# Optimization experiments

Measured on AMD Instinct MI355X. Metric: run time of the kernel, lower is better.

The kernel has to match this reference:

```python
import jax, jax.numpy as jnp
import numpy as np

N = 100000
E = 1600000
D_IN = 128
D_OUT = 128
EPS = 1e-5


def setup_inputs() -> dict:
    key = jax.random.key(0)
    ks = jax.random.split(key, 8)
    x = jax.random.normal(ks[0], (N, D_IN), dtype=jnp.float32)
    edge_index = jax.random.randint(ks[1], (2, E), 0, N, dtype=jnp.int64)
    s1 = 1.0 / np.sqrt(D_IN)
    s2 = 1.0 / np.sqrt(D_OUT)
    W1 = jax.random.uniform(ks[2], (D_IN, D_OUT), jnp.float32, -s1, s1)
    b1 = jax.random.uniform(ks[3], (D_OUT,), jnp.float32, -s1, s1)
    W2 = jax.random.uniform(ks[4], (D_OUT, D_OUT), jnp.float32, -s2, s2)
    b2 = jax.random.uniform(ks[5], (D_OUT,), jnp.float32, -s2, s2)
    gamma = jnp.ones((D_OUT,), jnp.float32)
    beta = jnp.zeros((D_OUT,), jnp.float32)
    return {"x": x, "edge_index": edge_index, "W1": W1, "b1": b1,
            "W2": W2, "b2": b2, "gamma": gamma, "beta": beta}


def reference(x, edge_index, W1, b1, W2, b2, gamma, beta):
    row, col = edge_index[0], edge_index[1]
    # scatter-add neighbor aggregation: agg[row] += x[col]
    agg = jax.ops.segment_sum(x[col], row, num_segments=N)
    h = x + agg  # residual (self) + aggregated neighbors
    # MLP: Linear -> ReLU -> Linear -> BatchNorm1d (training-mode batch stats)
    h = jax.nn.relu(h @ W1 + b1)
    h = h @ W2 + b2
    mean = jnp.mean(h, axis=0)
    var = jnp.mean(jnp.square(h - mean), axis=0)  # biased var, as torch BN uses
    out = gamma * (h - mean) * jax.lax.rsqrt(var + EPS) + beta
    return out
```

## Files before the change

### kernel.cpp

```cpp
#include <hip/hip_runtime.h>

#define N_NODES 100000
#define N_EDGES 1600000
#define DIM     128
#define EPS_BN  1e-5f
#define NB      512
#define NPB     196
#define EPB     3125
#define CAP     4096
#define M_TILE  64
#define M_PAD   100032
#define GBLK    1563
#define LPITCH  136

typedef __attribute__((ext_vector_type(8))) short short8;
typedef __attribute__((ext_vector_type(4))) float floatx4;

__device__ __forceinline__ unsigned short f2bf(float f) {
    unsigned u = __float_as_uint(f);
    return (unsigned short)((u + 0x7FFF + ((u >> 16) & 1)) >> 16);
}
__device__ __forceinline__ float bf2f(unsigned short b) {
    return __uint_as_float((unsigned)b << 16);
}

__device__ __forceinline__ int detect64(const void* eidx) {
    int v = ((const int*)eidx)[2 * (threadIdx.x & 63) + 1];
    unsigned long long b = __ballot(v != 0);
    return (b == 0ULL) ? 1 : 0;
}

__device__ __forceinline__ int load_row(const void* eidx, int is64, int e) {
    if (is64) return (int)((const long long*)eidx)[e];
    return ((const int*)eidx)[e];
}
__device__ __forceinline__ int load_col(const void* eidx, int is64, int e) {
    if (is64) return (int)((const long long*)eidx)[N_EDGES + e];
    return ((const int*)eidx)[N_EDGES + e];
}

__global__ __launch_bounds__(256) void bin_scatter(const void* eidx, int* bcur,
                                                   uint2* slots) {
    __shared__ int lh[NB];
    __shared__ int lbase[NB];
    for (int i = threadIdx.x; i < NB; i += 256) lh[i] = 0;
    int is64 = detect64(eidx);
    __syncthreads();
    int base = blockIdx.x * EPB;
    for (int i = threadIdx.x; i < EPB; i += 256) {
        int r = load_row(eidx, is64, base + i);
        atomicAdd(&lh[r / NPB], 1);
    }
    __syncthreads();
    for (int i = threadIdx.x; i < NB; i += 256) {
        int c = lh[i];
        lbase[i] = c ? atomicAdd(&bcur[i], c) : 0;
        lh[i] = 0;
    }
    __syncthreads();
    for (int i = threadIdx.x; i < EPB; i += 256) {
        int r = load_row(eidx, is64, base + i);
        int c = load_col(eidx, is64, base + i);
        int b = r / NPB;
        int pos = lbase[b] + atomicAdd(&lh[b], 1);
        slots[b * CAP + pos] = make_uint2((unsigned)r, (unsigned)c);
    }
}

__global__ void scan512(const int* bcnt, int* bstart, int* rowst) {
    __shared__ int tmp[NB];
    int t = threadIdx.x;
    int v = bcnt[t];
    tmp[t] = v;
    __syncthreads();
    for (int off = 1; off < NB; off <<= 1) {
        int a = (t >= off) ? tmp[t - off] : 0;
        __syncthreads();
        tmp[t] += a;
        __syncthreads();
    }
    bstart[t] = tmp[t] - v;
    if (t == NB - 1) { bstart[NB] = N_EDGES; rowst[N_NODES] = N_EDGES; }
}

__global__ __launch_bounds__(256) void build_csr(const uint2* __restrict__ slots,
                                                 const int* __restrict__ bstart,
                                                 int* __restrict__ rowst,
                                                 int* __restrict__ cols) {
    __shared__ int hist[256];
    __shared__ int excl[256];
    __shared__ int cur[256];
    __shared__ int colbuf[CAP];
    int b = blockIdx.x;
    int node0 = b * NPB;
    int nn = N_NODES - node0;
    if (nn <= 0) return;
    if (nn > NPB) nn = NPB;
    int s = bstart[b];
    int cnt = bstart[b + 1] - s;
    const uint2* pairs = slots + (size_t)b * CAP;
    int t = threadIdx.x;
    hist[t] = 0;
    __syncthreads();
    for (int i = t; i < cnt; i += 256)
        atomicAdd(&hist[(int)pairs[i].x - node0], 1);
    __syncthreads();
    int v = hist[t];
    excl[t] = v;
    __syncthreads();
    for (int off = 1; off < 256; off <<= 1) {
        int a = (t >= off) ? excl[t - off] : 0;
        __syncthreads();
        excl[t] += a;
        __syncthreads();
    }
    int ex = excl[t] - v;
    if (t < nn) rowst[node0 + t] = s + ex;
    cur[t] = ex;
    __syncthreads();
    if (cnt <= CAP) {
        for (int i = t; i < cnt; i += 256) {
            uint2 pr = pairs[i];
            int pos = atomicAdd(&cur[(int)pr.x - node0], 1);
            colbuf[pos] = (int)pr.y;
        }
        __syncthreads();
        for (int i = t; i < cnt; i += 256) cols[s + i] = colbuf[i];
    } else {
        for (int i = t; i < cnt; i += 256) {
            uint2 pr = pairs[i];
            int pos = atomicAdd(&cur[(int)pr.x - node0], 1);
            cols[s + pos] = (int)pr.y;
        }
    }
}

__global__ void xconv(const float* __restrict__ x,
                      unsigned short* __restrict__ xb) {
    int i = blockIdx.x * 256 + threadIdx.x;
    float4 v = ((const float4*)x)[i];
    ushort4 o;
    o.x = f2bf(v.x); o.y = f2bf(v.y); o.z = f2bf(v.z); o.w = f2bf(v.w);
    ((ushort4*)xb)[i] = o;
}

__global__ __launch_bounds__(256) void agg_kernel(
    const unsigned short* __restrict__ xb,
    const int* __restrict__ row_start, const int* __restrict__ cols,
    unsigned short* __restrict__ Hbf) {
    int wave = threadIdx.x >> 6;
    int lane = threadIdx.x & 63;
    int node = blockIdx.x * 4 + wave;
    const unsigned* xbw = (const unsigned*)xb;
    unsigned selfw = xbw[(size_t)node * 64 + lane];
    float2 acc;
    acc.x = __uint_as_float(selfw << 16);
    acc.y = __uint_as_float(selfw & 0xffff0000u);
    int s = row_start[node], e = row_start[node + 1];
    s = __builtin_amdgcn_readfirstlane(s);
    e = __builtin_amdgcn_readfirstlane(e);
    int j = s;
    for (; j + 16 <= e; j += 16) {
        unsigned pw[16];
#pragma unroll
        for (int u = 0; u < 16; ++u) {
            int c = cols[j + u];
            pw[u] = xbw[(size_t)c * 64 + lane];
        }
#pragma unroll
        for (int u = 0; u < 16; ++u) {
            acc.x += __uint_as_float(pw[u] << 16);
            acc.y += __uint_as_float(pw[u] & 0xffff0000u);
        }
    }
    for (; j + 4 <= e; j += 4) {
        unsigned pw[4];
#pragma unroll
        for (int u = 0; u < 4; ++u) {
            int c = cols[j + u];
            pw[u] = xbw[(size_t)c * 64 + lane];
        }
#pragma unroll
        for (int u = 0; u < 4; ++u) {
            acc.x += __uint_as_float(pw[u] << 16);
            acc.y += __uint_as_float(pw[u] & 0xffff0000u);
        }
    }
    for (; j < e; ++j) {
        unsigned p = xbw[(size_t)cols[j] * 64 + lane];
        acc.x += __uint_as_float(p << 16);
        acc.y += __uint_as_float(p & 0xffff0000u);
    }
    unsigned pack = (unsigned)f2bf(acc.x) | ((unsigned)f2bf(acc.y) << 16);
    ((unsigned*)Hbf)[(size_t)node * 64 + lane] = pack;
}

__global__ void convert_w(const float* __restrict__ W1,
                          const float* __restrict__ W2,
                          unsigned short* __restrict__ W1t,
                          unsigned short* __restrict__ W2t) {
    const float* W = blockIdx.x ? W2 : W1;
    unsigned short* Wt = blockIdx.x ? W2t : W1t;
    for (int i = threadIdx.x; i < DIM * DIM; i += 256) {
        int k = i >> 7, n = i & 127;
        Wt[n * DIM + k] = f2bf(W[i]);
    }
}

__global__ __launch_bounds__(256) void mlp_fused(
    const unsigned short* __restrict__ A,
    const unsigned short* __restrict__ B1t,
    const unsigned short* __restrict__ B2t,
    const float* __restrict__ bias1, const float* __restrict__ bias2,
    unsigned short* __restrict__ outb,
    float* __restrict__ gpart) {
    __shared__ unsigned short As[M_TILE * LPITCH];
    __shared__ unsigned short Bs[DIM * LPITCH];
    int t = threadIdx.x;
    int row0 = blockIdx.x * M_TILE;
    int lane = t & 63, wv = t >> 6;
    int m = lane & 15, g = lane >> 4;

#pragma unroll
    for (int i = 0; i < 4; ++i) {
        int ch = t + 256 * i;
        int r = ch >> 4, cc = ch & 15;
        *(uint4*)(&As[r * LPITCH + cc * 8]) =
            *(const uint4*)(&A[(size_t)(row0 + r) * DIM + cc * 8]);
    }
#pragma unroll
    for (int i = 0; i < 8; ++i) {
        int ch = t + 256 * i;
        int n = ch >> 4, cc = ch & 15;
        *(uint4*)(&Bs[n * LPITCH + cc * 8]) =
            *(const uint4*)(&B1t[n * DIM + cc * 8]);
    }
    __syncthreads();

    floatx4 acc1[8] = {};
#pragma unroll
    for (int kc = 0; kc < 4; ++kc) {
        short8 a = *(const short8*)(&As[(wv * 16 + m) * LPITCH + kc * 32 + g * 8]);
#pragma unroll
        for (int tt = 0; tt < 8; ++tt) {
            short8 b = *(const short8*)(&Bs[(tt * 16 + m) * LPITCH + kc * 32 + g * 8]);
            acc1[tt] = __builtin_amdgcn_mfma_f32_16x16x32_bf16(a, b, acc1[tt], 0, 0, 0);
        }
    }
    __syncthreads();

    uint4 wbuf[8];
#pragma unroll
    for (int i = 0; i < 8; ++i) {
        int ch = t + 256 * i;
        int n = ch >> 4, cc = ch & 15;
        wbuf[i] = *(const uint4*)(&B2t[n * DIM + cc * 8]);
    }
#pragma unroll
    for (int tt = 0; tt < 8; ++tt) {
        int col = tt * 16 + m;
        float bv = bias1[col];
#pragma unroll
        for (int j = 0; j < 4; ++j) {
            int rl = wv * 16 + g * 4 + j;
            As[rl * LPITCH + col] = f2bf(fmaxf(acc1[tt][j] + bv, 0.f));
        }
    }
#pragma unroll
    for (int i = 0; i < 8; ++i) {
        int ch = t + 256 * i;
        int n = ch >> 4, cc = ch & 15;
        *(uint4*)(&Bs[n * LPITCH + cc * 8]) = wbuf[i];
    }
    __syncthreads();

    floatx4 acc2[8] = {};
#pragma unroll
    for (int kc = 0; kc < 4; ++kc) {
        short8 a = *(const short8*)(&As[(wv * 16 + m) * LPITCH + kc * 32 + g * 8]);
#pragma unroll
        for (int tt = 0; tt < 8; ++tt) {
            short8 b = *(const short8*)(&Bs[(tt * 16 + m) * LPITCH + kc * 32 + g * 8]);
            acc2[tt] = __builtin_amdgcn_mfma_f32_16x16x32_bf16(a, b, acc2[tt], 0, 0, 0);
        }
    }

    float* csum = (float*)As;
    float* csq = csum + DIM;
    __syncthreads();
    if (t < DIM) { csum[t] = 0.f; csq[t] = 0.f; }
    __syncthreads();
#pragma unroll
    for (int tt = 0; tt < 8; ++tt) {
        int col = tt * 16 + m;
        float bv = bias2[col];
        float s = 0.f, q = 0.f;
#pragma unroll
        for (int j = 0; j < 4; ++j) {
            int row = row0 + wv * 16 + g * 4 + j;
            float v = acc2[tt][j] + bv;
            outb[(size_t)row * DIM + col] = f2bf(v);
            if (row < N_NODES) { s += v; q += v * v; }
        }
        atomicAdd(&csum[col], s);
        atomicAdd(&csq[col], q);
    }
    __syncthreads();
    gpart[(size_t)blockIdx.x * 256 + t] = (t < DIM) ? csum[t] : csq[t - DIM];
}

__global__ __launch_bounds__(256) void reduce_stats(
    const float* __restrict__ gpart, float* __restrict__ gstats) {
    int t = threadIdx.x;
    int chunk = (GBLK + 31) / 32;
    int r0 = blockIdx.x * chunk;
    int r1 = r0 + chunk < GBLK ? r0 + chunk : GBLK;
    float s = 0.f;
    for (int r = r0; r < r1; ++r) s += gpart[(size_t)r * 256 + t];
    atomicAdd(&gstats[t], s);
}

__global__ __launch_bounds__(256) void bn_apply(
    const unsigned short* __restrict__ H2, const float* __restrict__ gstats,
    const float* __restrict__ gamma, const float* __restrict__ beta,
    float* __restrict__ out) {
    __shared__ float sc_s[DIM], sh_s[DIM];
    int t = threadIdx.x;
    if (t < DIM) {
        float mean = gstats[t] * (1.0f / N_NODES);
        float m2 = gstats[DIM + t] * (1.0f / N_NODES);
        float var = m2 - mean * mean;
        float inv = rsqrtf(var + EPS_BN);
        float sc = gamma[t] * inv;
        sc_s[t] = sc;
        sh_s[t] = beta[t] - mean * sc;
    }
    __syncthreads();
    int i = blockIdx.x * 256 + t;
    int j4 = (i & 31) * 4;
    ushort4 hv = ((const ushort4*)H2)[i];
    float4 o;
    o.x = bf2f(hv.x) * sc_s[j4 + 0] + sh_s[j4 + 0];
    o.y = bf2f(hv.y) * sc_s[j4 + 1] + sh_s[j4 + 1];
    o.z = bf2f(hv.z) * sc_s[j4 + 2] + sh_s[j4 + 2];
    o.w = bf2f(hv.w) * sc_s[j4 + 3] + sh_s[j4 + 3];
    ((float4*)out)[i] = o;
}

extern "C" void kernel_launch(void* const* d_in, const int* in_sizes, int n_in,
                              void* d_out, int out_size, void* d_ws,
                              size_t ws_size, hipStream_t stream) {
    (void)in_sizes; (void)n_in; (void)out_size; (void)ws_size;
    const float* x     = (const float*)d_in[0];
    const void*  eidx  = d_in[1];
    const float* W1    = (const float*)d_in[2];
    const float* b1    = (const float*)d_in[3];
    const float* W2    = (const float*)d_in[4];
    const float* b2    = (const float*)d_in[5];
    const float* gamma = (const float*)d_in[6];
    const float* beta  = (const float*)d_in[7];
    float* out = (float*)d_out;

    char* p = (char*)d_ws;
    auto alloc = [&](size_t bytes) {
        char* r = p;
        p += (bytes + 255) & ~(size_t)255;
        return r;
    };
    unsigned short* Hbf  = (unsigned short*)alloc((size_t)M_PAD * DIM * 2);
    unsigned short* h2bf = (unsigned short*)alloc((size_t)M_PAD * DIM * 2);
    uint2* slots = (uint2*)h2bf;
    unsigned short* xb = (unsigned short*)alloc((size_t)N_NODES * DIM * 2);
    int*   cols   = (int*)alloc((size_t)N_EDGES * 4);
    float* gpart  = (float*)alloc((size_t)GBLK * 256 * 4);
    int*   rowst  = (int*)alloc((size_t)(N_NODES + 1) * 4);
    int*   bcur   = (int*)alloc(NB * 4);
    int*   bstart = (int*)alloc((NB + 1) * 4);
    unsigned short* W1t = (unsigned short*)alloc(DIM * DIM * 2);
    unsigned short* W2t = (unsigned short*)alloc(DIM * DIM * 2);
    float* gstats = (float*)alloc(2 * DIM * 4);

    hipMemsetAsync(bcur, 0, NB * 4, stream);
    hipMemsetAsync(gstats, 0, 2 * DIM * 4, stream);

    convert_w<<<2, 256, 0, stream>>>(W1, W2, W1t, W2t);
    bin_scatter<<<NB, 256, 0, stream>>>(eidx, bcur, slots);
    scan512<<<1, NB, 0, stream>>>(bcur, bstart, rowst);
    build_csr<<<NB, 256, 0, stream>>>(slots, bstart, rowst, cols);

    xconv<<<N_NODES * DIM / 4 / 256, 256, 0, stream>>>(x, xb);
    agg_kernel<<<N_NODES / 4, 256, 0, stream>>>(xb, rowst, cols, Hbf);

    mlp_fused<<<GBLK, 256, 0, stream>>>(Hbf, W1t, W2t, b1, b2, h2bf, gpart);
    reduce_stats<<<32, 256, 0, stream>>>(gpart, gstats);
    bn_apply<<<(N_NODES * DIM / 4) / 256, 256, 0, stream>>>(h2bf, gstats,
                                                            gamma, beta, out);
}
```

Measured before the change: 325.6 us.

## Pack edge slots, stage bin scatter in LDS, fold scan and memsets into kernels

The two memsets move into the weight-conversion kernel and the separate 512-bin scan is folded into build_csr, so fewer kernels are launched. bin_scatter now uses half as many blocks, each handling twice the edges, and sorts its edges by bin in shared memory before writing, which makes the global stores more contiguous. Each (row, col) pair is packed into one 32-bit word with the local row in the top 8 bits, halving slot traffic. The aggregation kernel gets branch-free 16- and 32-wide unrolled paths for low-degree nodes. Risks: the build_csr fallback for cnt > CAP is dropped, the 24-bit column packing assumes N_NODES fits in 24 bits, and the large LDS staging arrays can lower occupancy.

```diff
diff --git a/kernel.cpp b/kernel.cpp
--- a/kernel.cpp
+++ b/kernel.cpp
@@ -6,7 +6,8 @@
 #define EPS_BN  1e-5f
 #define NB      512
 #define NPB     196
-#define EPB     3125
+#define NBLK    256
+#define EPB     6250
 #define CAP     4096
 #define M_TILE  64
 #define M_PAD   100032
@@ -29,7 +30,6 @@
     unsigned long long b = __ballot(v != 0);
     return (b == 0ULL) ? 1 : 0;
 }
-
 __device__ __forceinline__ int load_row(const void* eidx, int is64, int e) {
     if (is64) return (int)((const long long*)eidx)[e];
     return ((const int*)eidx)[e];
@@ -39,71 +39,107 @@
     return ((const int*)eidx)[N_EDGES + e];
 }
 
+__global__ void convert_w(const float* __restrict__ W1,
+                          const float* __restrict__ W2,
+                          unsigned short* __restrict__ W1t,
+                          unsigned short* __restrict__ W2t,
+                          int* __restrict__ bcur, float* __restrict__ gstats) {
+    if (blockIdx.x == 2) {
+        int t = threadIdx.x;
+        if (t < NB) bcur[t] = 0;
+        if (t < 256) { if (t < NB - 256) bcur[256 + t] = 0; }
+        bcur[256 + threadIdx.x] = 0;
+        if (t < 2 * DIM) gstats[t] = 0.f;
+        return;
+    }
+    const float* W = blockIdx.x ? W2 : W1;
+    unsigned short* Wt = blockIdx.x ? W2t : W1t;
+    for (int i = threadIdx.x; i < DIM * DIM; i += 256) {
+        int k = i >> 7, n = i & 127;
+        Wt[n * DIM + k] = f2bf(W[i]);
+    }
+}
+
 __global__ __launch_bounds__(256) void bin_scatter(const void* eidx, int* bcur,
-                                                   uint2* slots) {
+                                                   unsigned* __restrict__ slots) {
     __shared__ int lh[NB];
     __shared__ int lbase[NB];
-    for (int i = threadIdx.x; i < NB; i += 256) lh[i] = 0;
+    __shared__ int loff[NB];
+    __shared__ unsigned stage[EPB];
+    __shared__ int gaddr[EPB];
+    int t = threadIdx.x;
     int is64 = detect64(eidx);
+    lh[t] = 0; lh[t + 256] = 0;
     __syncthreads();
     int base = blockIdx.x * EPB;
-    for (int i = threadIdx.x; i < EPB; i += 256) {
+    for (int i = t; i < EPB; i += 256) {
         int r = load_row(eidx, is64, base + i);
         atomicAdd(&lh[r / NPB], 1);
     }
     __syncthreads();
-    for (int i = threadIdx.x; i < NB; i += 256) {
+    loff[t] = lh[t]; loff[t + 256] = lh[t + 256];
+    __syncthreads();
+    for (int off = 1; off < NB; off <<= 1) {
+        int a0 = (t >= off) ? loff[t - off] : 0;
+        int a1 = (t + 256 >= off) ? loff[t + 256 - off] : 0;
+        __syncthreads();
+        loff[t] += a0; loff[t + 256] += a1;
+        __syncthreads();
+    }
+#pragma unroll
+    for (int q = 0; q < 2; ++q) {
+        int i = t + 256 * q;
         int c = lh[i];
         lbase[i] = c ? atomicAdd(&bcur[i], c) : 0;
+        loff[i] -= c;
         lh[i] = 0;
     }
     __syncthreads();
-    for (int i = threadIdx.x; i < EPB; i += 256) {
+    for (int i = t; i < EPB; i += 256) {
         int r = load_row(eidx, is64, base + i);
         int c = load_col(eidx, is64, base + i);
         int b = r / NPB;
-        int pos = lbase[b] + atomicAdd(&lh[b], 1);
-        slots[b * CAP + pos] = make_uint2((unsigned)r, (unsigned)c);
-    }
-}
-
-__global__ void scan512(const int* bcnt, int* bstart, int* rowst) {
-    __shared__ int tmp[NB];
-    int t = threadIdx.x;
-    int v = bcnt[t];
-    tmp[t] = v;
-    __syncthreads();
-    for (int off = 1; off < NB; off <<= 1) {
-        int a = (t >= off) ? tmp[t - off] : 0;
-        __syncthreads();
-        tmp[t] += a;
-        __syncthreads();
-    }
-    bstart[t] = tmp[t] - v;
-    if (t == NB - 1) { bstart[NB] = N_EDGES; rowst[N_NODES] = N_EDGES; }
-}
-
-__global__ __launch_bounds__(256) void build_csr(const uint2* __restrict__ slots,
-                                                 const int* __restrict__ bstart,
+        int pos = atomicAdd(&lh[b], 1);
+        int idx = loff[b] + pos;
+        stage[idx] = ((unsigned)(r - b * NPB) << 24) | (unsigned)c;
+        gaddr[idx] = b * CAP + lbase[b] + pos;
+    }
+    __syncthreads();
+    for (int i = t; i < EPB; i += 256)
+        slots[gaddr[i]] = stage[i];
+}
+
+__global__ __launch_bounds__(256) void build_csr(const unsigned* __restrict__ slots,
+                                                 const int* __restrict__ bcnt,
                                                  int* __restrict__ rowst,
                                                  int* __restrict__ cols) {
+    __shared__ int tmp[NB];
     __shared__ int hist[256];
     __shared__ int excl[256];
     __shared__ int cur[256];
     __shared__ int colbuf[CAP];
+    int t = threadIdx.x;
     int b = blockIdx.x;
+    tmp[t] = bcnt[t]; tmp[t + 256] = bcnt[t + 256];
+    __syncthreads();
+    for (int off = 1; off < NB; off <<= 1) {
+        int a0 = (t >= off) ? tmp[t - off] : 0;
+        int a1 = (t + 256 >= off) ? tmp[t + 256 - off] : 0;
+        __syncthreads();
+        tmp[t] += a0; tmp[t + 256] += a1;
+        __syncthreads();
+    }
+    int cnt = bcnt[b];
+    int s = tmp[b] - cnt;
     int node0 = b * NPB;
     int nn = N_NODES - node0;
-    if (nn <= 0) return;
     if (nn > NPB) nn = NPB;
-    int s = bstart[b];
-    int cnt = bstart[b + 1] - s;
-    const uint2* pairs = slots + (size_t)b * CAP;
-    int t = threadIdx.x;
+    const unsigned* pairs = slots + (size_t)b * CAP;
     hist[t] = 0;
+    if (b == NB - 1 && t == 0) rowst[N_NODES] = N_EDGES;
     __syncthreads();
     for (int i = t; i < cnt; i += 256)
-        atomicAdd(&hist[(int)pairs[i].x - node0], 1);
+        atomicAdd(&hist[(int)(pairs[i] >> 24)], 1);
     __syncthreads();
     int v = hist[t];
     excl[t] = v;
@@ -118,21 +154,13 @@
     if (t < nn) rowst[node0 + t] = s + ex;
     cur[t] = ex;
     __syncthreads();
-    if (cnt <= CAP) {
-        for (int i = t; i < cnt; i += 256) {
-            uint2 pr = pairs[i];
-            int pos = atomicAdd(&cur[(int)pr.x - node0], 1);
-            colbuf[pos] = (int)pr.y;
-        }
-        __syncthreads();
-        for (int i = t; i < cnt; i += 256) cols[s + i] = colbuf[i];
-    } else {
-        for (int i = t; i < cnt; i += 256) {
-            uint2 pr = pairs[i];
-            int pos = atomicAdd(&cur[(int)pr.x - node0], 1);
-            cols[s + pos] = (int)pr.y;
-        }
-    }
+    for (int i = t; i < cnt; i += 256) {
+        unsigned pr = pairs[i];
+        int pos = atomicAdd(&cur[pr >> 24], 1);
+        colbuf[pos] = (int)(pr & 0xFFFFFFu);
+    }
+    __syncthreads();
+    for (int i = t; i < cnt; i += 256) cols[s + i] = colbuf[i];
 }
 
 __global__ void xconv(const float* __restrict__ x,
@@ -159,52 +187,56 @@
     int s = row_start[node], e = row_start[node + 1];
     s = __builtin_amdgcn_readfirstlane(s);
     e = __builtin_amdgcn_readfirstlane(e);
-    int j = s;
-    for (; j + 16 <= e; j += 16) {
+    int d = e - s;
+    if (d <= 16) {
         unsigned pw[16];
 #pragma unroll
         for (int u = 0; u < 16; ++u) {
-            int c = cols[j + u];
-            pw[u] = xbw[(size_t)c * 64 + lane];
+            int idx = s + u;
+            int ci = (idx < e) ? idx : s;
+            pw[u] = xbw[(size_t)cols[ci] * 64 + lane];
         }
 #pragma unroll
         for (int u = 0; u < 16; ++u) {
-            acc.x += __uint_as_float(pw[u] << 16);
-            acc.y += __uint_as_float(pw[u] & 0xffff0000u);
-        }
-    }
-    for (; j + 4 <= e; j += 4) {
-        unsigned pw[4];
-#pragma unroll
-        for (int u = 0; u < 4; ++u) {
-            int c = cols[j + u];
-            pw[u] = xbw[(size_t)c * 64 + lane];
-        }
-#pragma unroll
-        for (int u = 0; u < 4; ++u) {
-            acc.x += __uint_as_float(pw[u] << 16);
-            acc.y += __uint_as_float(pw[u] & 0xffff0000u);
-        }
-    }
-    for (; j < e; ++j) {
-        unsigned p = xbw[(size_t)cols[j] * 64 + lane];
-        acc.x += __uint_as_float(p << 16);
-        acc.y += __uint_as_float(p & 0xffff0000u);
+            unsigned w = (u < d) ? pw[u] : 0u;
+            acc.x += __uint_as_float(w << 16);
+            acc.y += __uint_as_float(w & 0xffff0000u);
+        }
+    } else if (d <= 32) {
+        unsigned pw[32];
+#pragma unroll
+        for (int u = 0; u < 32; ++u) {
+            int idx = s + u;
+            int ci = (idx < e) ? idx : s;
+            pw[u] = xbw[(size_t)cols[ci] * 64 + lane];
+        }
+#pragma unroll
+        for (int u = 0; u < 32; ++u) {
+            unsigned w = (u < d) ? pw[u] : 0u;
+            acc.x += __uint_as_float(w << 16);
+            acc.y += __uint_as_float(w & 0xffff0000u);
+        }
+    } else {
+        int j = s;
+        for (; j + 16 <= e; j += 16) {
+            unsigned pw[16];
+#pragma unroll
+            for (int u = 0; u < 16; ++u)
+                pw[u] = xbw[(size_t)cols[j + u] * 64 + lane];
+#pragma unroll
+            for (int u = 0; u < 16; ++u) {
+                acc.x += __uint_as_float(pw[u] << 16);
+                acc.y += __uint_as_float(pw[u] & 0xffff0000u);
+            }
+        }
+        for (; j < e; ++j) {
+            unsigned pv = xbw[(size_t)cols[j] * 64 + lane];
+            acc.x += __uint_as_float(pv << 16);
+            acc.y += __uint_as_float(pv & 0xffff0000u);
+        }
     }
     unsigned pack = (unsigned)f2bf(acc.x) | ((unsigned)f2bf(acc.y) << 16);
     ((unsigned*)Hbf)[(size_t)node * 64 + lane] = pack;
-}
-
-__global__ void convert_w(const float* __restrict__ W1,
-                          const float* __restrict__ W2,
-                          unsigned short* __restrict__ W1t,
-                          unsigned short* __restrict__ W2t) {
-    const float* W = blockIdx.x ? W2 : W1;
-    unsigned short* Wt = blockIdx.x ? W2t : W1t;
-    for (int i = threadIdx.x; i < DIM * DIM; i += 256) {
-        int k = i >> 7, n = i & 127;
-        Wt[n * DIM + k] = f2bf(W[i]);
-    }
 }
 
 __global__ __launch_bounds__(256) void mlp_fused(
@@ -369,24 +401,19 @@
     };
     unsigned short* Hbf  = (unsigned short*)alloc((size_t)M_PAD * DIM * 2);
     unsigned short* h2bf = (unsigned short*)alloc((size_t)M_PAD * DIM * 2);
-    uint2* slots = (uint2*)h2bf;
+    unsigned* slots = (unsigned*)h2bf;
     unsigned short* xb = (unsigned short*)alloc((size_t)N_NODES * DIM * 2);
-    int*   cols   = (int*)alloc((size_t)N_EDGES * 4);
+    int*   cols   = (int*)alloc((size_t)(N_EDGES + 64) * 4);
     float* gpart  = (float*)alloc((size_t)GBLK * 256 * 4);
     int*   rowst  = (int*)alloc((size_t)(N_NODES + 1) * 4);
     int*   bcur   = (int*)alloc(NB * 4);
-    int*   bstart = (int*)alloc((NB + 1) * 4);
     unsigned short* W1t = (unsigned short*)alloc(DIM * DIM * 2);
     unsigned short* W2t = (unsigned short*)alloc(DIM * DIM * 2);
     float* gstats = (float*)alloc(2 * DIM * 4);
 
-    hipMemsetAsync(bcur, 0, NB * 4, stream);
-    hipMemsetAsync(gstats, 0, 2 * DIM * 4, stream);
-
-    convert_w<<<2, 256, 0, stream>>>(W1, W2, W1t, W2t);
-    bin_scatter<<<NB, 256, 0, stream>>>(eidx, bcur, slots);
-    scan512<<<1, NB, 0, stream>>>(bcur, bstart, rowst);
-    build_csr<<<NB, 256, 0, stream>>>(slots, bstart, rowst, cols);
+    convert_w<<<3, 256, 0, stream>>>(W1, W2, W1t, W2t, bcur, gstats);
+    bin_scatter<<<NBLK, 256, 0, stream>>>(eidx, bcur, slots);
+    build_csr<<<NB, 256, 0, stream>>>(slots, bcur, rowst, cols);
 
     xconv<<<N_NODES * DIM / 4 / 256, 256, 0, stream>>>(x, xb);
     agg_kernel<<<N_NODES / 4, 256, 0, stream>>>(xb, rowst, cols, Hbf);
```

Measured after the change: 310.8 us. 1.05x faster.
